# Kernel optimization log

Measured on AMD Instinct MI355X. Metric: run time of the kernel, lower is better.

The kernel has to match this reference:

```python
import jax, jax.numpy as jnp
import numpy as np

B, T, V, E, H, C = 64, 512, 32000, 256, 512, 4

def setup_inputs() -> dict:
    key = jax.random.key(0)
    ks = jax.random.split(key, 8)
    s = 1.0 / np.sqrt(H)  # torch LSTM default init scale
    return {
        "x": jax.random.randint(ks[0], (B, T), 0, V),
        "emb": jax.random.normal(ks[1], (V, E), jnp.float32) * 0.1,
        "W_ih": jax.random.uniform(ks[2], (4 * H, E), jnp.float32, -s, s),
        "W_hh": jax.random.uniform(ks[3], (4 * H, H), jnp.float32, -s, s),
        "b_ih": jax.random.uniform(ks[4], (4 * H,), jnp.float32, -s, s),
        "b_hh": jax.random.uniform(ks[5], (4 * H,), jnp.float32, -s, s),
        "W_fc": jax.random.uniform(ks[6], (C, H), jnp.float32, -s, s),
        "b_fc": jax.random.uniform(ks[7], (C,), jnp.float32, -s, s),
    }

def _lstm_last_hidden(e, W_ih, W_hh, b_ih, b_hh):
    # e: [B,T,E]. Precompute input-side gate preactivations for all steps.
    xg = jnp.einsum('bte,ge->tbg', e, W_ih) + (b_ih + b_hh)  # [T,B,4H]
    h0 = jnp.zeros((e.shape[0], H), e.dtype)
    c0 = jnp.zeros((e.shape[0], H), e.dtype)

    def step(carry, xt):
        h, c = carry
        g = xt + h @ W_hh.T                       # [B,4H]
        i, f, gg, o = jnp.split(g, 4, axis=-1)    # torch gate order: i,f,g,o
        i = jax.nn.sigmoid(i)
        f = jax.nn.sigmoid(f)
        gg = jnp.tanh(gg)
        o = jax.nn.sigmoid(o)
        c = f * c + i * gg
        h = o * jnp.tanh(c)
        return (h, c), None

    (hT, _), _ = jax.lax.scan(step, (h0, c0), xg)
    return hT  # last hidden == lstm_out[:, -1, :] for unidirectional LSTM

def reference(x, emb, W_ih, W_hh, b_ih, b_hh, W_fc, b_fc):
    e = emb[x]                                    # [B,T,E] embedding lookup
    hT = _lstm_last_hidden(e, W_ih, W_hh, b_ih, b_hh)
    return hT @ W_fc.T + b_fc                     # [B,C] logits
```

## Files before the change

kernel.cpp:

```cpp
#include <hip/hip_runtime.h>
#include <hip/hip_bf16.h>

#define B_  64
#define T_  512
#define E_  256
#define H_  512
#define G4_ 2048
#define C_  4

typedef __attribute__((ext_vector_type(4))) float  f32x4;
typedef __attribute__((ext_vector_type(8))) __bf16 bf16x8;
typedef __attribute__((ext_vector_type(8))) short  short8;
typedef __attribute__((ext_vector_type(4))) short  s16x4;

union V16 { f32x4 f; bf16x8 b; short8 s; };

__device__ __forceinline__ float sigmoid_(float x) { return 1.0f / (1.0f + __expf(-x)); }
__device__ __forceinline__ float tanh_(float x)    { return 1.0f - 2.0f / (__expf(2.0f * x) + 1.0f); }

__device__ __forceinline__ short f2bf(float f) {
  union { float f; unsigned u; } v; v.f = f;
  return (short)((v.u + 0x7FFFu + ((v.u >> 16) & 1u)) >> 16);
}

__device__ __forceinline__ void store_short_llc(void* p, unsigned v) {
  asm volatile("global_store_short %0, %1, off sc0 sc1" :: "v"(p), "v"(v) : "memory");
}
__device__ __forceinline__ void store_dword_llc(void* p, float v) {
  asm volatile("global_store_dword %0, %1, off sc0 sc1" :: "v"(p), "v"(v) : "memory");
}
__device__ __forceinline__ void load2_dwordx4_llc(const void* p0, const void* p1,
                                                  f32x4* a, f32x4* b) {
  asm volatile(
      "global_load_dwordx4 %0, %2, off sc0 sc1\n\t"
      "global_load_dwordx4 %1, %3, off sc0 sc1\n\t"
      "s_waitcnt vmcnt(0)"
      : "=&v"(*a), "=&v"(*b) : "v"(p0), "v"(p1) : "memory");
}

__global__ __launch_bounds__(256, 1) void xg_kernel(
    const int* __restrict__ x, const float* __restrict__ emb,
    const float* __restrict__ W_ih,
    __hip_bfloat16* __restrict__ xg)
{
  const int t   = blockIdx.x;
  const int tid = threadIdx.x;
  __shared__ int s_idx[B_];
  __shared__ __hip_bfloat16 s_e[B_][E_ + 8];

  if (tid < B_) s_idx[tid] = x[tid * T_ + t];
  __syncthreads();
  {
    int b = tid >> 2, ch = tid & 3;
    const float* src = emb + (size_t)s_idx[b] * E_ + ch * 64;
    short* dst = (short*)&s_e[b][ch * 64];
#pragma unroll
    for (int i = 0; i < 16; i++) {
      f32x4 v = *(const f32x4*)(src + i * 4);
      s16x4 s;
      s[0] = f2bf(v[0]); s[1] = f2bf(v[1]); s[2] = f2bf(v[2]); s[3] = f2bf(v[3]);
      *(s16x4*)(dst + i * 4) = s;
    }
  }
  __syncthreads();

  const int wv   = tid >> 6;
  const int lane = tid & 63;
  const int ln15 = lane & 15, quad = lane >> 4;

  V16 breg[4][8];
#pragma unroll
  for (int nt = 0; nt < 4; nt++)
#pragma unroll
    for (int ks = 0; ks < 8; ks++)
      breg[nt][ks].f = *(const f32x4*)(&s_e[nt * 16 + ln15][quad * 8 + ks * 32]);

  const int gbase = wv * 512;
  const size_t base_t = (size_t)t * (G4_ * B_);
  for (int mt = 0; mt < 32; mt++) {
    const int grow = gbase + mt * 16 + ln15;
    const float* arow = W_ih + (size_t)grow * E_ + quad * 8;
    V16 areg[8];
#pragma unroll
    for (int ks = 0; ks < 8; ks++) {
      f32x4 lo = *(const f32x4*)(arow + ks * 32);
      f32x4 hi = *(const f32x4*)(arow + ks * 32 + 4);
      short8 s;
      s[0] = f2bf(lo[0]); s[1] = f2bf(lo[1]); s[2] = f2bf(lo[2]); s[3] = f2bf(lo[3]);
      s[4] = f2bf(hi[0]); s[5] = f2bf(hi[1]); s[6] = f2bf(hi[2]); s[7] = f2bf(hi[3]);
      areg[ks].s = s;
    }

    f32x4 acc[4];
#pragma unroll
    for (int nt = 0; nt < 4; nt++) acc[nt] = (f32x4){0.f, 0.f, 0.f, 0.f};
#pragma unroll
    for (int ks = 0; ks < 8; ks++)
#pragma unroll
      for (int nt = 0; nt < 4; nt++)
        acc[nt] = __builtin_amdgcn_mfma_f32_16x16x32_bf16(areg[ks].b, breg[nt][ks].b, acc[nt], 0, 0, 0);

    const int mrow0 = gbase + mt * 16 + quad * 4;
#pragma unroll
    for (int nt = 0; nt < 4; nt++) {
      const int batch = nt * 16 + ln15;
#pragma unroll
      for (int r = 0; r < 4; r++) {
        const int grow2 = mrow0 + r;
        const int d = grow2 & 511;
        short sv = f2bf(acc[nt][r]);
        *((short*)xg + base_t + ((size_t)wv << 15) + ((size_t)batch << 9) + d) = sv;
      }
    }
  }
}

__global__ __launch_bounds__(512, 2) void lstm_kernel(
    const float* __restrict__ W_hh,
    const float* __restrict__ b_ih, const float* __restrict__ b_hh,
    const float* __restrict__ W_fc, const float* __restrict__ b_fc,
    const __hip_bfloat16* __restrict__ xg,
    unsigned int* flags, __hip_bfloat16* hbuf , float* hT,
    float* out)
{
  const int tid  = threadIdx.x;
  const int blk  = blockIdx.x;
  const int pb   = blk & 3;
  const int pd   = blk >> 2;
  const int d0   = pd * 32;
  const int wv   = tid >> 6;
  const int lane = tid & 63;
  const int ln15 = lane & 15, quad = lane >> 4;

  __shared__ __hip_bfloat16 s_h[16][520];
  __shared__ float s_pre[4][16][36];

  V16 areg[16];
  {
    const int grow = (wv >> 1) * 512 + d0 + (wv & 1) * 16 + ln15;
    const float* ap = W_hh + (size_t)grow * H_ + quad * 8;
#pragma unroll
    for (int ks = 0; ks < 16; ks++) {
      f32x4 lo = *(const f32x4*)(ap + ks * 32);
      f32x4 hi = *(const f32x4*)(ap + ks * 32 + 4);
      short8 s;
      s[0] = f2bf(lo[0]); s[1] = f2bf(lo[1]); s[2] = f2bf(lo[2]); s[3] = f2bf(lo[3]);
      s[4] = f2bf(hi[0]); s[5] = f2bf(hi[1]); s[6] = f2bf(hi[2]); s[7] = f2bf(hi[3]);
      areg[ks].s = s;
    }
  }

  const int nb = tid >> 5;
  const int nd = tid & 31;
  const int gb = pb * 16 + nb;
  const int dg = d0 + nd;
  const float bias_i = b_ih[dg]        + b_hh[dg];
  const float bias_f = b_ih[512 + dg]  + b_hh[512 + dg];
  const float bias_g = b_ih[1024 + dg] + b_hh[1024 + dg];
  const float bias_o = b_ih[1536 + dg] + b_hh[1536 + dg];
  float c = 0.0f;
  const int myflag = pb * 16 + pd;

  for (int t = 0; t < T_; t++) {
    const int cur = t & 1, nxt = cur ^ 1;

    const size_t xoff = (size_t)t * (G4_ * B_) + ((size_t)gb << 9) + dg;
    const __hip_bfloat16 xgi = xg[xoff];
    const __hip_bfloat16 xgf = xg[xoff + (1u << 15)];
    const __hip_bfloat16 xgg = xg[xoff + (2u << 15)];
    const __hip_bfloat16 xgo = xg[xoff + (3u << 15)];

    if (tid < 16) {
      const unsigned* fp = flags + pb * 16 + tid;
      while (__hip_atomic_load(fp, __ATOMIC_RELAXED, __HIP_MEMORY_SCOPE_AGENT) < (unsigned)t) {}
    }
    __syncthreads();

    {
      const short* hbase = (const short*)hbuf + (size_t)cur * (B_ * H_) + (size_t)(pb * 16) * H_;
      const int i0 = tid, i1 = tid + 512;
      f32x4 va, vb;
      load2_dwordx4_llc(hbase + i0 * 8, hbase + i1 * 8, &va, &vb);
      *(f32x4*)&s_h[i0 >> 6][(i0 & 63) * 8] = va;
      *(f32x4*)&s_h[i1 >> 6][(i1 & 63) * 8] = vb;
    }
    __syncthreads();

    f32x4 acc0 = (f32x4){0.f, 0.f, 0.f, 0.f};
    f32x4 acc1 = (f32x4){0.f, 0.f, 0.f, 0.f};
#pragma unroll
    for (int ks = 0; ks < 16; ks += 2) {
      V16 b0, b1;
      b0.f = *(const f32x4*)&s_h[ln15][quad * 8 + ks * 32];
      b1.f = *(const f32x4*)&s_h[ln15][quad * 8 + (ks + 1) * 32];
      acc0 = __builtin_amdgcn_mfma_f32_16x16x32_bf16(areg[ks].b,     b0.b, acc0, 0, 0, 0);
      acc1 = __builtin_amdgcn_mfma_f32_16x16x32_bf16(areg[ks + 1].b, b1.b, acc1, 0, 0, 0);
    }
    const f32x4 accs = acc0 + acc1;

    *(f32x4*)&s_pre[wv >> 1][ln15][(wv & 1) * 16 + quad * 4] = accs;
    __syncthreads();

    {
      const float pi = s_pre[0][nb][nd] + bias_i + __bfloat162float(xgi);
      const float pf = s_pre[1][nb][nd] + bias_f + __bfloat162float(xgf);
      const float pg = s_pre[2][nb][nd] + bias_g + __bfloat162float(xgg);
      const float po = s_pre[3][nb][nd] + bias_o + __bfloat162float(xgo);
      const float i_ = sigmoid_(pi), f_ = sigmoid_(pf);
      const float g_ = tanh_(pg),    o_ = sigmoid_(po);
      c = f_ * c + i_ * g_;
      const float h = o_ * tanh_(c);
      if (t < T_ - 1) {
        short* hp = (short*)hbuf + (size_t)nxt * (B_ * H_) + (size_t)gb * H_ + dg;
        store_short_llc(hp, (unsigned)(unsigned short)f2bf(h));
      } else {
        store_dword_llc(hT + gb * H_ + dg, h);
      }
    }
    __syncthreads();

    if (tid == 0)
      __hip_atomic_store(&flags[myflag], (unsigned)(t + 1),
                         __ATOMIC_RELAXED, __HIP_MEMORY_SCOPE_AGENT);
  }

  if (blk == 0) {
    if (tid < 64)
      while (__hip_atomic_load(&flags[tid], __ATOMIC_RELAXED, __HIP_MEMORY_SCOPE_AGENT) < (unsigned)T_) {}
    __builtin_amdgcn_fence(__ATOMIC_ACQUIRE, "agent");
    __syncthreads();
    for (int o = tid; o < B_ * C_; o += 512) {
      const int b = o >> 2, cl = o & 3;
      const f32x4* hr = (const f32x4*)(hT + b * H_);
      const f32x4* wr = (const f32x4*)(W_fc + cl * H_);
      float s = 0.f;
      for (int d4 = 0; d4 < H_ / 4; d4++) {
        const f32x4 hv = hr[d4];
        const f32x4 wv4 = wr[d4];
        s += hv[0] * wv4[0] + hv[1] * wv4[1] + hv[2] * wv4[2] + hv[3] * wv4[3];
      }
      s += b_fc[cl];
      out[o] = s;
    }
  }
}

extern "C" void kernel_launch(void* const* d_in, const int* in_sizes, int n_in,
                              void* d_out, int out_size, void* d_ws, size_t ws_size,
                              hipStream_t stream) {
  const int*   x    = (const int*)d_in[0];
  const float* emb  = (const float*)d_in[1];
  const float* W_ih = (const float*)d_in[2];
  const float* W_hh = (const float*)d_in[3];
  const float* b_ih = (const float*)d_in[4];
  const float* b_hh = (const float*)d_in[5];
  const float* W_fc = (const float*)d_in[6];
  const float* b_fc = (const float*)d_in[7];
  float* out = (float*)d_out;

  char* ws = (char*)d_ws;
  const size_t XG_OFF = 524288;
  const size_t NEEDED = XG_OFF + (size_t)T_ * G4_ * B_ * 2;
  if (ws_size < NEEDED) return;

  unsigned int*   flags = (unsigned int*)ws;
  __hip_bfloat16* hbuf  = (__hip_bfloat16*)(ws + 4096);
  float*          hT    = (float*)(ws + 135168);
  __hip_bfloat16* xg    = (__hip_bfloat16*)(ws + XG_OFF);

  (void)hipMemsetAsync(ws, 0, 135168, stream);

  xg_kernel<<<T_, 256, 0, stream>>>(x, emb, W_ih, xg);
  lstm_kernel<<<64, 512, 0, stream>>>(W_hh, b_ih, b_hh, W_fc, b_fc, xg,
                                      flags, hbuf, hT, out);
}
```

Baseline: 1.469 ms.

## Replace per-step flag barrier with step-tagged hidden-state words polled directly

Each hidden value is now stored as a 32-bit word that packs the bf16 h with the step number, so consumers poll the data buffer itself until every tag matches, instead of waiting on per-block flags. This removes the extra __syncthreads, the flag store and the separate flag-poll round trip from each recurrent step. The cost is twice the hidden-state traffic, repeated wide polling loads, and a 16-bit tag compare that relies on T<65536. The xg kernel output store is also vectorized to 4-element bf16 writes.

Result: slower. 1.617 ms (+10.1%).

```diff
diff --git a/kernel.cpp b/kernel.cpp
--- a/kernel.cpp
+++ b/kernel.cpp
@@ -12,6 +12,8 @@
 typedef __attribute__((ext_vector_type(8))) __bf16 bf16x8;
 typedef __attribute__((ext_vector_type(8))) short  short8;
 typedef __attribute__((ext_vector_type(4))) short  s16x4;
+typedef __attribute__((ext_vector_type(4))) unsigned int u32x4;
+typedef __attribute__((ext_vector_type(2))) unsigned int u32x2;
 
 union V16 { f32x4 f; bf16x8 b; short8 s; };
 
@@ -23,19 +25,24 @@
   return (short)((v.u + 0x7FFFu + ((v.u >> 16) & 1u)) >> 16);
 }
 
-__device__ __forceinline__ void store_short_llc(void* p, unsigned v) {
-  asm volatile("global_store_short %0, %1, off sc0 sc1" :: "v"(p), "v"(v) : "memory");
-}
-__device__ __forceinline__ void store_dword_llc(void* p, float v) {
+__device__ __forceinline__ void store_u32_llc(void* p, unsigned v) {
   asm volatile("global_store_dword %0, %1, off sc0 sc1" :: "v"(p), "v"(v) : "memory");
 }
-__device__ __forceinline__ void load2_dwordx4_llc(const void* p0, const void* p1,
-                                                  f32x4* a, f32x4* b) {
+__device__ __forceinline__ void store_f32_llc(void* p, float v) {
+  asm volatile("global_store_dword %0, %1, off sc0 sc1" :: "v"(p), "v"(v) : "memory");
+}
+__device__ __forceinline__ void load4x16_llc(const void* q0, const void* q1,
+                                             const void* q2, const void* q3,
+                                             u32x4* a, u32x4* b, u32x4* c, u32x4* d) {
   asm volatile(
-      "global_load_dwordx4 %0, %2, off sc0 sc1\n\t"
-      "global_load_dwordx4 %1, %3, off sc0 sc1\n\t"
+      "global_load_dwordx4 %0, %4, off sc0 sc1\n\t"
+      "global_load_dwordx4 %1, %5, off sc0 sc1\n\t"
+      "global_load_dwordx4 %2, %6, off sc0 sc1\n\t"
+      "global_load_dwordx4 %3, %7, off sc0 sc1\n\t"
       "s_waitcnt vmcnt(0)"
-      : "=&v"(*a), "=&v"(*b) : "v"(p0), "v"(p1) : "memory");
+      : "=&v"(*a), "=&v"(*b), "=&v"(*c), "=&v"(*d)
+      : "v"(q0), "v"(q1), "v"(q2), "v"(q3)
+      : "memory");
 }
 
 __global__ __launch_bounds__(256, 1) void xg_kernel(
@@ -100,17 +107,14 @@
       for (int nt = 0; nt < 4; nt++)
         acc[nt] = __builtin_amdgcn_mfma_f32_16x16x32_bf16(areg[ks].b, breg[nt][ks].b, acc[nt], 0, 0, 0);
 
-    const int mrow0 = gbase + mt * 16 + quad * 4;
+    const int dbase = mt * 16 + quad * 4;
 #pragma unroll
     for (int nt = 0; nt < 4; nt++) {
       const int batch = nt * 16 + ln15;
-#pragma unroll
-      for (int r = 0; r < 4; r++) {
-        const int grow2 = mrow0 + r;
-        const int d = grow2 & 511;
-        short sv = f2bf(acc[nt][r]);
-        *((short*)xg + base_t + ((size_t)wv << 15) + ((size_t)batch << 9) + d) = sv;
-      }
+      s16x4 sv;
+#pragma unroll
+      for (int r = 0; r < 4; r++) sv[r] = f2bf(acc[nt][r]);
+      *(s16x4*)((short*)xg + base_t + ((size_t)wv << 15) + ((size_t)batch << 9) + dbase) = sv;
     }
   }
 }
@@ -120,7 +124,7 @@
     const float* __restrict__ b_ih, const float* __restrict__ b_hh,
     const float* __restrict__ W_fc, const float* __restrict__ b_fc,
     const __hip_bfloat16* __restrict__ xg,
-    unsigned int* flags, __hip_bfloat16* hbuf , float* hT,
+    unsigned int* flags, unsigned int* hbuf2 , float* hT,
     float* out)
 {
   const int tid  = threadIdx.x;
@@ -159,10 +163,12 @@
   const float bias_g = b_ih[1024 + dg] + b_hh[1024 + dg];
   const float bias_o = b_ih[1536 + dg] + b_hh[1536 + dg];
   float c = 0.0f;
-  const int myflag = pb * 16 + pd;
+
+  const int srow = tid >> 7;
+  const int scol = (tid * 4) & 511;
 
   for (int t = 0; t < T_; t++) {
-    const int cur = t & 1, nxt = cur ^ 1;
+    const int cur = t & 1;
 
     const size_t xoff = (size_t)t * (G4_ * B_) + ((size_t)gb << 9) + dg;
     const __hip_bfloat16 xgi = xg[xoff];
@@ -170,19 +176,34 @@
     const __hip_bfloat16 xgg = xg[xoff + (2u << 15)];
     const __hip_bfloat16 xgo = xg[xoff + (3u << 15)];
 
-    if (tid < 16) {
-      const unsigned* fp = flags + pb * 16 + tid;
-      while (__hip_atomic_load(fp, __ATOMIC_RELAXED, __HIP_MEMORY_SCOPE_AGENT) < (unsigned)t) {}
-    }
-    __syncthreads();
-
+    const unsigned* wb = hbuf2 + (size_t)cur * (B_ * H_) +
+                         (size_t)(pb * 16) * H_ + tid * 4;
+    u32x4 a0, a1, a2, a3;
     {
-      const short* hbase = (const short*)hbuf + (size_t)cur * (B_ * H_) + (size_t)(pb * 16) * H_;
-      const int i0 = tid, i1 = tid + 512;
-      f32x4 va, vb;
-      load2_dwordx4_llc(hbase + i0 * 8, hbase + i1 * 8, &va, &vb);
-      *(f32x4*)&s_h[i0 >> 6][(i0 & 63) * 8] = va;
-      *(f32x4*)&s_h[i1 >> 6][(i1 & 63) * 8] = vb;
+      const unsigned tg = (unsigned)t;
+      while (true) {
+        load4x16_llc(wb, wb + 2048, wb + 4096, wb + 6144, &a0, &a1, &a2, &a3);
+        unsigned m = (a0[0] ^ tg) | (a0[1] ^ tg) | (a0[2] ^ tg) | (a0[3] ^ tg)
+                   | (a1[0] ^ tg) | (a1[1] ^ tg) | (a1[2] ^ tg) | (a1[3] ^ tg)
+                   | (a2[0] ^ tg) | (a2[1] ^ tg) | (a2[2] ^ tg) | (a2[3] ^ tg)
+                   | (a3[0] ^ tg) | (a3[1] ^ tg) | (a3[2] ^ tg) | (a3[3] ^ tg);
+        if ((m & 0xFFFFu) == 0) break;
+      }
+    }
+    {
+      u32x2 v;
+      v[0] = (a0[0] >> 16) | (a0[1] & 0xFFFF0000u);
+      v[1] = (a0[2] >> 16) | (a0[3] & 0xFFFF0000u);
+      *(u32x2*)&s_h[srow][scol] = v;
+      v[0] = (a1[0] >> 16) | (a1[1] & 0xFFFF0000u);
+      v[1] = (a1[2] >> 16) | (a1[3] & 0xFFFF0000u);
+      *(u32x2*)&s_h[srow + 4][scol] = v;
+      v[0] = (a2[0] >> 16) | (a2[1] & 0xFFFF0000u);
+      v[1] = (a2[2] >> 16) | (a2[3] & 0xFFFF0000u);
+      *(u32x2*)&s_h[srow + 8][scol] = v;
+      v[0] = (a3[0] >> 16) | (a3[1] & 0xFFFF0000u);
+      v[1] = (a3[2] >> 16) | (a3[3] & 0xFFFF0000u);
+      *(u32x2*)&s_h[srow + 12][scol] = v;
     }
     __syncthreads();
 
@@ -211,18 +232,19 @@
       c = f_ * c + i_ * g_;
       const float h = o_ * tanh_(c);
       if (t < T_ - 1) {
-        short* hp = (short*)hbuf + (size_t)nxt * (B_ * H_) + (size_t)gb * H_ + dg;
-        store_short_llc(hp, (unsigned)(unsigned short)f2bf(h));
+        const unsigned w = ((unsigned)(unsigned short)f2bf(h) << 16) | (unsigned)(t + 1);
+        store_u32_llc(hbuf2 + (size_t)(cur ^ 1) * (B_ * H_) + (size_t)gb * H_ + dg, w);
       } else {
-        store_dword_llc(hT + gb * H_ + dg, h);
+        store_f32_llc(hT + gb * H_ + dg, h);
       }
     }
-    __syncthreads();
-
-    if (tid == 0)
-      __hip_atomic_store(&flags[myflag], (unsigned)(t + 1),
-                         __ATOMIC_RELAXED, __HIP_MEMORY_SCOPE_AGENT);
-  }
+  }
+
+  asm volatile("s_waitcnt vmcnt(0)" ::: "memory");
+  __syncthreads();
+  if (tid == 0)
+    __hip_atomic_store(&flags[blk], (unsigned)T_,
+                       __ATOMIC_RELAXED, __HIP_MEMORY_SCOPE_AGENT);
 
   if (blk == 0) {
     if (tid < 64)
@@ -259,18 +281,18 @@
   float* out = (float*)d_out;
 
   char* ws = (char*)d_ws;
-  const size_t XG_OFF = 524288;
+  const size_t XG_OFF = 397312;
   const size_t NEEDED = XG_OFF + (size_t)T_ * G4_ * B_ * 2;
   if (ws_size < NEEDED) return;
 
   unsigned int*   flags = (unsigned int*)ws;
-  __hip_bfloat16* hbuf  = (__hip_bfloat16*)(ws + 4096);
-  float*          hT    = (float*)(ws + 135168);
+  unsigned int*   hbuf2 = (unsigned int*)(ws + 4096);
+  float*          hT    = (float*)(ws + 266240);
   __hip_bfloat16* xg    = (__hip_bfloat16*)(ws + XG_OFF);
 
-  (void)hipMemsetAsync(ws, 0, 135168, stream);
+  (void)hipMemsetAsync(ws, 0, 266240, stream);
 
   xg_kernel<<<T_, 256, 0, stream>>>(x, emb, W_ih, xg);
   lstm_kernel<<<64, 512, 0, stream>>>(W_hh, b_ih, b_hh, W_fc, b_fc, xg,
-                                      flags, hbuf, hT, out);
-}
+                                      flags, hbuf2, hT, out);
+}
```

## Regroup LSTM blocks into 8-batch groups with fine-grained per-wave flags and xg prefetch

Applied to the files above, without the earlier changes.

The LSTM blocks are reorganized into 8 batch groups with 64 hidden units each, using 1024 threads per block. Half the MFMA rows are zero padding. Each wave now publishes its own flag right after storing its h slice, and consumers poll only the flags covering the rows they load. This replaces the per-block flag that required a full barrier before it was set. The next step's xg gate inputs are prefetched asynchronously during the current step, and the xg writes become vectorized 4-element stores. The cost is wasted MFMA work on the padded rows and many more flag polls per step.

After: 3.302 ms. 2.25x slower.

```diff
diff --git a/kernel.cpp b/kernel.cpp
--- a/kernel.cpp
+++ b/kernel.cpp
@@ -23,19 +23,38 @@
   return (short)((v.u + 0x7FFFu + ((v.u >> 16) & 1u)) >> 16);
 }
 
-__device__ __forceinline__ void store_short_llc(void* p, unsigned v) {
+__device__ __forceinline__ void st_u16_llc(void* p, unsigned v) {
   asm volatile("global_store_short %0, %1, off sc0 sc1" :: "v"(p), "v"(v) : "memory");
 }
-__device__ __forceinline__ void store_dword_llc(void* p, float v) {
+__device__ __forceinline__ void st_u32_llc(void* p, unsigned v) {
   asm volatile("global_store_dword %0, %1, off sc0 sc1" :: "v"(p), "v"(v) : "memory");
 }
-__device__ __forceinline__ void load2_dwordx4_llc(const void* p0, const void* p1,
-                                                  f32x4* a, f32x4* b) {
+__device__ __forceinline__ void st_f32_llc(void* p, float v) {
+  asm volatile("global_store_dword %0, %1, off sc0 sc1" :: "v"(p), "v"(v) : "memory");
+}
+__device__ __forceinline__ unsigned ld_u32_llc(const void* p) {
+  unsigned v;
+  asm volatile("global_load_dword %0, %1, off sc0 sc1\n\ts_waitcnt vmcnt(0)"
+               : "=&v"(v) : "v"(p) : "memory");
+  return v;
+}
+__device__ __forceinline__ f32x4 ld_b128_llc(const void* p) {
+  f32x4 v;
+  asm volatile("global_load_dwordx4 %0, %1, off sc0 sc1\n\ts_waitcnt vmcnt(0)"
+               : "=&v"(v) : "v"(p) : "memory");
+  return v;
+}
+__device__ __forceinline__ void prefetch_xg(const short* p,
+                                            unsigned* r0, unsigned* r1,
+                                            unsigned* r2, unsigned* r3) {
   asm volatile(
-      "global_load_dwordx4 %0, %2, off sc0 sc1\n\t"
-      "global_load_dwordx4 %1, %3, off sc0 sc1\n\t"
-      "s_waitcnt vmcnt(0)"
-      : "=&v"(*a), "=&v"(*b) : "v"(p0), "v"(p1) : "memory");
+      "global_load_ushort %0, %4, off\n\t"
+      "global_load_ushort %1, %5, off\n\t"
+      "global_load_ushort %2, %6, off\n\t"
+      "global_load_ushort %3, %7, off"
+      : "=&v"(*r0), "=&v"(*r1), "=&v"(*r2), "=&v"(*r3)
+      : "v"(p), "v"(p + 32768), "v"(p + 65536), "v"(p + 98304)
+      : "memory");
 }
 
 __global__ __launch_bounds__(256, 1) void xg_kernel(
@@ -100,44 +119,41 @@
       for (int nt = 0; nt < 4; nt++)
         acc[nt] = __builtin_amdgcn_mfma_f32_16x16x32_bf16(areg[ks].b, breg[nt][ks].b, acc[nt], 0, 0, 0);
 
-    const int mrow0 = gbase + mt * 16 + quad * 4;
+    const int dbase = mt * 16 + quad * 4;
 #pragma unroll
     for (int nt = 0; nt < 4; nt++) {
       const int batch = nt * 16 + ln15;
-#pragma unroll
-      for (int r = 0; r < 4; r++) {
-        const int grow2 = mrow0 + r;
-        const int d = grow2 & 511;
-        short sv = f2bf(acc[nt][r]);
-        *((short*)xg + base_t + ((size_t)wv << 15) + ((size_t)batch << 9) + d) = sv;
-      }
-    }
-  }
-}
-
-__global__ __launch_bounds__(512, 2) void lstm_kernel(
+      s16x4 sv;
+#pragma unroll
+      for (int r = 0; r < 4; r++) sv[r] = f2bf(acc[nt][r]);
+      *(s16x4*)((short*)xg + base_t + ((size_t)wv << 15) + ((size_t)batch << 9) + dbase) = sv;
+    }
+  }
+}
+
+__global__ __launch_bounds__(1024, 4) void lstm_kernel(
     const float* __restrict__ W_hh,
     const float* __restrict__ b_ih, const float* __restrict__ b_hh,
     const float* __restrict__ W_fc, const float* __restrict__ b_fc,
     const __hip_bfloat16* __restrict__ xg,
-    unsigned int* flags, __hip_bfloat16* hbuf , float* hT,
+    unsigned int* ctl, __hip_bfloat16* hbuf , float* hT,
     float* out)
 {
   const int tid  = threadIdx.x;
   const int blk  = blockIdx.x;
-  const int pb   = blk & 3;
-  const int pd   = blk >> 2;
-  const int d0   = pd * 32;
+  const int g    = blk & 7;
+  const int pd   = blk >> 3;
+  const int d0   = pd * 64;
   const int wv   = tid >> 6;
   const int lane = tid & 63;
   const int ln15 = lane & 15, quad = lane >> 4;
 
   __shared__ __hip_bfloat16 s_h[16][520];
-  __shared__ float s_pre[4][16][36];
+  __shared__ float s_pre[4][8][68];
 
   V16 areg[16];
   {
-    const int grow = (wv >> 1) * 512 + d0 + (wv & 1) * 16 + ln15;
+    const int grow = (wv >> 2) * 512 + d0 + (wv & 3) * 16 + ln15;
     const float* ap = W_hh + (size_t)grow * H_ + quad * 8;
 #pragma unroll
     for (int ks = 0; ks < 16; ks++) {
@@ -150,39 +166,38 @@
     }
   }
 
-  const int nb = tid >> 5;
-  const int nd = tid & 31;
-  const int gb = pb * 16 + nb;
+  const int nb = tid >> 6;
+  const int nd = tid & 63;
+  const int gb = g * 8 + nb;
   const int dg = d0 + nd;
-  const float bias_i = b_ih[dg]        + b_hh[dg];
-  const float bias_f = b_ih[512 + dg]  + b_hh[512 + dg];
-  const float bias_g = b_ih[1024 + dg] + b_hh[1024 + dg];
-  const float bias_o = b_ih[1536 + dg] + b_hh[1536 + dg];
+  float bias_i = 0.f, bias_f = 0.f, bias_g = 0.f, bias_o = 0.f;
+  if (tid < 512) {
+    bias_i = b_ih[dg]        + b_hh[dg];
+    bias_f = b_ih[512 + dg]  + b_hh[512 + dg];
+    bias_g = b_ih[1024 + dg] + b_hh[1024 + dg];
+    bias_o = b_ih[1536 + dg] + b_hh[1536 + dg];
+  } else {
+    const int i2 = tid - 512;
+    *(f32x4*)&s_h[8 + (i2 >> 6)][(i2 & 63) * 8] = (f32x4){0.f, 0.f, 0.f, 0.f};
+  }
   float c = 0.0f;
-  const int myflag = pb * 16 + pd;
+
+  const short* xg_s = (const short*)xg;
+  unsigned px0 = 0, px1 = 0, px2 = 0, px3 = 0;
+  if (tid < 512)
+    prefetch_xg(xg_s + ((size_t)gb << 9) + dg, &px0, &px1, &px2, &px3);
+
+  __syncthreads();
 
   for (int t = 0; t < T_; t++) {
-    const int cur = t & 1, nxt = cur ^ 1;
-
-    const size_t xoff = (size_t)t * (G4_ * B_) + ((size_t)gb << 9) + dg;
-    const __hip_bfloat16 xgi = xg[xoff];
-    const __hip_bfloat16 xgf = xg[xoff + (1u << 15)];
-    const __hip_bfloat16 xgg = xg[xoff + (2u << 15)];
-    const __hip_bfloat16 xgo = xg[xoff + (3u << 15)];
-
-    if (tid < 16) {
-      const unsigned* fp = flags + pb * 16 + tid;
-      while (__hip_atomic_load(fp, __ATOMIC_RELAXED, __HIP_MEMORY_SCOPE_AGENT) < (unsigned)t) {}
-    }
-    __syncthreads();
-
-    {
-      const short* hbase = (const short*)hbuf + (size_t)cur * (B_ * H_) + (size_t)(pb * 16) * H_;
-      const int i0 = tid, i1 = tid + 512;
-      f32x4 va, vb;
-      load2_dwordx4_llc(hbase + i0 * 8, hbase + i1 * 8, &va, &vb);
-      *(f32x4*)&s_h[i0 >> 6][(i0 & 63) * 8] = va;
-      *(f32x4*)&s_h[i1 >> 6][(i1 & 63) * 8] = vb;
+    const int cur = t & 1;
+
+    if (tid < 512) {
+      const unsigned* fp = ctl + g * 64 + ((tid & 63) >> 3) * 8 + nb;
+      while (ld_u32_llc(fp) < (unsigned)t) {}
+      f32x4 hv = ld_b128_llc((const short*)hbuf + (size_t)cur * (B_ * H_) +
+                             (size_t)(g * 8) * H_ + tid * 8);
+      *(f32x4*)&s_h[nb][(tid & 63) * 8] = hv;
     }
     __syncthreads();
 
@@ -198,39 +213,46 @@
     }
     const f32x4 accs = acc0 + acc1;
 
-    *(f32x4*)&s_pre[wv >> 1][ln15][(wv & 1) * 16 + quad * 4] = accs;
+    if (ln15 < 8)
+      *(f32x4*)&s_pre[wv >> 2][ln15][(wv & 3) * 16 + quad * 4] = accs;
     __syncthreads();
 
-    {
-      const float pi = s_pre[0][nb][nd] + bias_i + __bfloat162float(xgi);
-      const float pf = s_pre[1][nb][nd] + bias_f + __bfloat162float(xgf);
-      const float pg = s_pre[2][nb][nd] + bias_g + __bfloat162float(xgg);
-      const float po = s_pre[3][nb][nd] + bias_o + __bfloat162float(xgo);
+    if (tid < 512) {
+      const float pi = s_pre[0][nb][nd] + bias_i + __uint_as_float(px0 << 16);
+      const float pf = s_pre[1][nb][nd] + bias_f + __uint_as_float(px1 << 16);
+      const float pg = s_pre[2][nb][nd] + bias_g + __uint_as_float(px2 << 16);
+      const float po = s_pre[3][nb][nd] + bias_o + __uint_as_float(px3 << 16);
       const float i_ = sigmoid_(pi), f_ = sigmoid_(pf);
       const float g_ = tanh_(pg),    o_ = sigmoid_(po);
       c = f_ * c + i_ * g_;
       const float h = o_ * tanh_(c);
       if (t < T_ - 1) {
-        short* hp = (short*)hbuf + (size_t)nxt * (B_ * H_) + (size_t)gb * H_ + dg;
-        store_short_llc(hp, (unsigned)(unsigned short)f2bf(h));
+        st_u16_llc((short*)hbuf + (size_t)(cur ^ 1) * (B_ * H_) + (size_t)gb * H_ + dg,
+                   (unsigned)(unsigned short)f2bf(h));
+        asm volatile("s_waitcnt vmcnt(0)" ::: "memory");
+        if ((tid & 63) == 0)
+          st_u32_llc(ctl + g * 64 + pd * 8 + nb, (unsigned)(t + 1));
       } else {
-        store_dword_llc(hT + gb * H_ + dg, h);
+        st_f32_llc(hT + gb * H_ + dg, h);
       }
-    }
-    __syncthreads();
-
-    if (tid == 0)
-      __hip_atomic_store(&flags[myflag], (unsigned)(t + 1),
-                         __ATOMIC_RELAXED, __HIP_MEMORY_SCOPE_AGENT);
-  }
+      const int tt = (t + 1 < T_) ? t + 1 : 0;
+      prefetch_xg(xg_s + (size_t)tt * (G4_ * B_) + ((size_t)gb << 9) + dg,
+                  &px0, &px1, &px2, &px3);
+    }
+  }
+
+  asm volatile("s_waitcnt vmcnt(0)" ::: "memory");
+  __syncthreads();
+  if (tid == 0)
+    __hip_atomic_store(ctl + 576 + blk, 1u, __ATOMIC_RELAXED, __HIP_MEMORY_SCOPE_AGENT);
 
   if (blk == 0) {
     if (tid < 64)
-      while (__hip_atomic_load(&flags[tid], __ATOMIC_RELAXED, __HIP_MEMORY_SCOPE_AGENT) < (unsigned)T_) {}
+      while (__hip_atomic_load(ctl + 576 + tid, __ATOMIC_RELAXED, __HIP_MEMORY_SCOPE_AGENT) < 1u) {}
     __builtin_amdgcn_fence(__ATOMIC_ACQUIRE, "agent");
     __syncthreads();
-    for (int o = tid; o < B_ * C_; o += 512) {
-      const int b = o >> 2, cl = o & 3;
+    if (tid < B_ * C_) {
+      const int b = tid >> 2, cl = tid & 3;
       const f32x4* hr = (const f32x4*)(hT + b * H_);
       const f32x4* wr = (const f32x4*)(W_fc + cl * H_);
       float s = 0.f;
@@ -240,7 +262,7 @@
         s += hv[0] * wv4[0] + hv[1] * wv4[1] + hv[2] * wv4[2] + hv[3] * wv4[3];
       }
       s += b_fc[cl];
-      out[o] = s;
+      out[tid] = s;
     }
   }
 }
@@ -259,18 +281,18 @@
   float* out = (float*)d_out;
 
   char* ws = (char*)d_ws;
-  const size_t XG_OFF = 524288;
+  const size_t XG_OFF = 397312;
   const size_t NEEDED = XG_OFF + (size_t)T_ * G4_ * B_ * 2;
   if (ws_size < NEEDED) return;
 
-  unsigned int*   flags = (unsigned int*)ws;
-  __hip_bfloat16* hbuf  = (__hip_bfloat16*)(ws + 4096);
-  float*          hT    = (float*)(ws + 135168);
-  __hip_bfloat16* xg    = (__hip_bfloat16*)(ws + XG_OFF);
-
-  (void)hipMemsetAsync(ws, 0, 135168, stream);
+  unsigned int*   ctl  = (unsigned int*)ws;
+  __hip_bfloat16* hbuf = (__hip_bfloat16*)(ws + 4096);
+  float*          hT   = (float*)(ws + 135168);
+  __hip_bfloat16* xg   = (__hip_bfloat16*)(ws + XG_OFF);
+
+  (void)hipMemsetAsync(ws, 0, 266240, stream);
 
   xg_kernel<<<T_, 256, 0, stream>>>(x, emb, W_ih, xg);
-  lstm_kernel<<<64, 512, 0, stream>>>(W_hh, b_ih, b_hh, W_fc, b_fc, xg,
-                                      flags, hbuf, hT, out);
-}
+  lstm_kernel<<<64, 1024, 0, stream>>>(W_hh, b_ih, b_hh, W_fc, b_fc, xg,
+                                       ctl, hbuf, hT, out);
+}
```
